# Performance work log

Hardware: AMD Instinct MI355X
Metric: run time of the kernel (lower is better)

## Reference

```python
import jax, jax.numpy as jnp
import numpy as np


def setup_inputs() -> dict:
    key = jax.random.key(0)
    ks = jax.random.split(key, 7)
    B, N, D, A = 32, 128, 512, 512
    sD = 1.0 / np.sqrt(D)
    sA = 1.0 / np.sqrt(A)
    return {
        "x": jax.random.normal(ks[0], (B, N, D), dtype=jnp.float32),
        "W1": jax.random.normal(ks[1], (A, D), dtype=jnp.float32) * sD,
        "b1": jax.random.normal(ks[2], (A,), dtype=jnp.float32) * sD,
        "W2": jax.random.normal(ks[3], (A, D), dtype=jnp.float32) * sD,
        "b2": jax.random.normal(ks[4], (A,), dtype=jnp.float32) * sD,
        "Wout": jax.random.normal(ks[5], (A,), dtype=jnp.float32) * sA,
        "bout": jax.random.normal(ks[6], (1,), dtype=jnp.float32) * sA,
    }


def reference(x, W1, b1, W2, b2, Wout, bout):
    # x: (B, N, D)
    x1 = jnp.einsum('bnd,ad->bna', x, W1) + b1  # mlp1 -> (B, N, A)
    x2 = jnp.einsum('bnd,ad->bna', x, W2) + b2  # mlp2 -> (B, N, A)
    # outer broadcast add: x1.unsqueeze(1) + x2.unsqueeze(2) -> (B, N, N, A)
    s = x1[:, None, :, :] + x2[:, :, None, :]
    # include_root=False: drop ROOT row along dim 1 -> (B, N-1, N, A)
    s = s[:, 1:, :, :]
    s = jnp.tanh(s)
    # out linear A -> 1, then squeeze -> (B, N-1, N)
    return jnp.einsum('bija,a->bij', s, Wout) + bout[0]
```

## Files before the change

### kernel.cpp

```cpp
#include <hip/hip_runtime.h>
#include <hip/hip_bf16.h>

#define B_ 32
#define N_ 128
#define D_ 512
#define A_ 512
#define R_ (B_*N_)
#define OC 1024
#define CEXP 2.8853900817779268f

typedef __attribute__((ext_vector_type(8)))  short frag_ab;
typedef __attribute__((ext_vector_type(16))) float frag_c;

__device__ inline unsigned pack2bf(float a, float b) {
    unsigned ua = __builtin_bit_cast(unsigned, a) + 0x8000u;
    unsigned ub = __builtin_bit_cast(unsigned, b) + 0x8000u;
    return __builtin_amdgcn_perm(ub, ua, 0x07060302);
}
__device__ inline float bf2f_lo(unsigned u){ return __builtin_bit_cast(float, u << 16); }
__device__ inline float bf2f_hi(unsigned u){ return __builtin_bit_cast(float, u & 0xffff0000u); }

__global__ __launch_bounds__(256) void k0_cvt(
    const float* __restrict__ X, const float* __restrict__ W1,
    const float* __restrict__ W2,
    unsigned short* __restrict__ Xb, unsigned short* __restrict__ W1b,
    unsigned short* __restrict__ W2b)
{
    const int NX = R_*D_/8, NW = A_*D_/8;
    int i = blockIdx.x*256 + threadIdx.x;
    const float* src; unsigned short* dst; int off;
    if (i < NX)            { src = X;  dst = Xb;  off = i; }
    else if (i < NX+NW)    { src = W1; dst = W1b; off = i-NX; }
    else if (i < NX+2*NW)  { src = W2; dst = W2b; off = i-NX-NW; }
    else return;
    float4 a = ((const float4*)src)[off*2];
    float4 c = ((const float4*)src)[off*2+1];
    uint4 o;
    o.x = pack2bf(a.x,a.y); o.y = pack2bf(a.z,a.w);
    o.z = pack2bf(c.x,c.y); o.w = pack2bf(c.z,c.w);
    ((uint4*)dst)[off] = o;
}

#define LDK1 36

__global__ __launch_bounds__(256) void k1_mfma(
    const unsigned short* __restrict__ Xb,
    const unsigned short* __restrict__ W1b, const float* __restrict__ b1,
    const unsigned short* __restrict__ W2b, const float* __restrict__ b2,
    unsigned short* __restrict__ Yb)
{
    __shared__ unsigned short As[2][128*LDK1];
    __shared__ unsigned short Bs[2][128*LDK1];

    const int t = threadIdx.x, lane = t&63, wid = t>>6;
    const int wr = wid>>1, wc = wid&1;
    const int row0 = blockIdx.x*128, col0 = blockIdx.y*128;
    const unsigned short* Wb = (col0 < A_) ? W1b : W2b;
    const float* bb = (col0 < A_) ? b1 : b2;
    const int wrow0 = col0 & (A_-1);

    const int srow = t>>1;
    const int scol = (t&1)*16;

    frag_c acc[2][2];
#pragma unroll
    for (int i=0;i<2;++i)
#pragma unroll
        for (int j=0;j<2;++j)
#pragma unroll
            for (int r=0;r<16;++r) acc[i][j][r] = 0.f;

    const int fr = lane & 31;
    const int ko = (lane >> 5) * 8;

    {
        const unsigned short* px = &Xb[(size_t)(row0 +srow)*D_ + scol];
        const unsigned short* pw = &Wb[(size_t)(wrow0+srow)*D_ + scol];
        uint4 a0 = *(const uint4*)px, a1 = *(const uint4*)(px+8);
        uint4 b0 = *(const uint4*)pw, b1v = *(const uint4*)(pw+8);
        *(uint4*)&As[0][srow*LDK1 + scol]     = a0;
        *(uint4*)&As[0][srow*LDK1 + scol + 8] = a1;
        *(uint4*)&Bs[0][srow*LDK1 + scol]     = b0;
        *(uint4*)&Bs[0][srow*LDK1 + scol + 8] = b1v;
    }
    __syncthreads();

#pragma unroll
    for (int s = 0; s < 16; ++s) {
        const int cur = s & 1;
        uint4 a0, a1, b0, b1v;
        if (s < 15) {
            const int k0 = (s+1)*32;
            const unsigned short* px = &Xb[(size_t)(row0 +srow)*D_ + k0 + scol];
            const unsigned short* pw = &Wb[(size_t)(wrow0+srow)*D_ + k0 + scol];
            a0 = *(const uint4*)px; a1 = *(const uint4*)(px+8);
            b0 = *(const uint4*)pw; b1v = *(const uint4*)(pw+8);
        }
        frag_ab af[2][2], bf[2][2];
#pragma unroll
        for (int mt=0; mt<2; ++mt)
#pragma unroll
            for (int ks=0; ks<2; ++ks) {
                af[mt][ks] = *(const frag_ab*)&As[cur][(wr*64+mt*32+fr)*LDK1 + ks*16 + ko];
                bf[mt][ks] = *(const frag_ab*)&Bs[cur][(wc*64+mt*32+fr)*LDK1 + ks*16 + ko];
            }
#pragma unroll
        for (int ks=0; ks<2; ++ks)
#pragma unroll
            for (int mt=0; mt<2; ++mt)
#pragma unroll
                for (int nt=0; nt<2; ++nt)
                    acc[mt][nt] = __builtin_amdgcn_mfma_f32_32x32x16_bf16(
                        af[mt][ks], bf[nt][ks], acc[mt][nt], 0, 0, 0);
        if (s < 15) {
            *(uint4*)&As[cur^1][srow*LDK1 + scol]     = a0;
            *(uint4*)&As[cur^1][srow*LDK1 + scol + 8] = a1;
            *(uint4*)&Bs[cur^1][srow*LDK1 + scol]     = b0;
            *(uint4*)&Bs[cur^1][srow*LDK1 + scol + 8] = b1v;
        }
        __syncthreads();
    }

#pragma unroll
    for (int mt=0; mt<2; ++mt) {
        const int rbase = row0 + wr*64 + mt*32 + 4*(lane>>5);
#pragma unroll
        for (int nt=0; nt<2; ++nt) {
            const int cc = col0 + wc*64 + nt*32 + (lane&31);
            const float bias = bb[cc & (A_-1)];
#pragma unroll
            for (int r=0; r<16; ++r) {
                const int rr = rbase + (r&3) + 8*(r>>2);
                float e = __builtin_amdgcn_exp2f(CEXP*(acc[mt][nt][r] + bias));
                Yb[(size_t)rr*OC + cc] =
                    (unsigned short)((__builtin_bit_cast(unsigned, e) + 0x8000u) >> 16);
            }
        }
    }
}

#define LDW 132

__device__ inline int swz(int r, int c) { return r*LDW + (c ^ (((r>>2)&7)<<2)); }

__global__ __launch_bounds__(256) void k2_tanh(
    const unsigned short* __restrict__ Yb,
    const float* __restrict__ Wout, const float* __restrict__ bout,
    float* __restrict__ out)
{
    __shared__ float e1s[64*LDW];
    __shared__ float e2s[64*LDW];
    __shared__ float wo[128];
    __shared__ float wsum_s[4];

    const int t  = threadIdx.x;
    const int jt = blockIdx.x & 1;
    const int it = blockIdx.x >> 1;
    const int ah = blockIdx.y;
    const int b  = blockIdx.z;
    const int abase = ah << 7;

    {
        float w = (t < 128) ? Wout[abase + t] : 0.f;
        if (t < 128) wo[t] = w;
#pragma unroll
        for (int off=32; off>=1; off>>=1) w += __shfl_down(w, off, 64);
        if ((t&63)==0) wsum_s[t>>6] = w;
    }

    const unsigned short* yb = Yb + (size_t)b*N_*OC;
    const int sr = t>>4;
    const int sc = (t&15)*8;

#pragma unroll
    for (int q=0; q<4; ++q) {
        const int r = q*16 + sr;
        uint4 v1 = *(const uint4*)&yb[(size_t)(jt*64 + r)*OC + abase + sc];
        int i2 = it*64 + r + 1; if (i2 > 127) i2 = 127;
        uint4 v2 = *(const uint4*)&yb[(size_t)i2*OC + A_ + abase + sc];
        *(float4*)&e1s[swz(r, sc)]   = float4{bf2f_lo(v1.x),bf2f_hi(v1.x),bf2f_lo(v1.y),bf2f_hi(v1.y)};
        *(float4*)&e1s[swz(r, sc+4)] = float4{bf2f_lo(v1.z),bf2f_hi(v1.z),bf2f_lo(v1.w),bf2f_hi(v1.w)};
        *(float4*)&e2s[swz(r, sc)]   = float4{bf2f_lo(v2.x),bf2f_hi(v2.x),bf2f_lo(v2.y),bf2f_hi(v2.y)};
        *(float4*)&e2s[swz(r, sc+4)] = float4{bf2f_lo(v2.z),bf2f_hi(v2.z),bf2f_lo(v2.w),bf2f_hi(v2.w)};
    }
    __syncthreads();

    const int jl = t&15, il = t>>4;
    float acc[4][4];
#pragma unroll
    for (int kj=0;kj<4;++kj)
#pragma unroll
        for (int ki=0;ki<4;++ki) acc[kj][ki] = 0.f;

#pragma unroll 1
    for (int c=0; c<128; c+=4) {
        float4 u[4], v[4];
#pragma unroll
        for (int kj=0;kj<4;++kj) u[kj] = *(const float4*)&e1s[swz(4*jl+kj, c)];
#pragma unroll
        for (int ki=0;ki<4;++ki) v[ki] = *(const float4*)&e2s[swz(4*il+ki, c)];
        float4 w4 = *(const float4*)&wo[c];
#pragma unroll
        for (int kj=0;kj<4;++kj)
#pragma unroll
            for (int ki=0;ki<4;++ki) {
                float r0 = fmaf(u[kj].x, v[ki].x, 1.f);
                float s0 = fmaf(u[kj].y, v[ki].y, 1.f);
                acc[kj][ki] = fmaf(fmaf(w4.x, s0, w4.y*r0),
                                   __builtin_amdgcn_rcpf(r0*s0), acc[kj][ki]);
                float r1 = fmaf(u[kj].z, v[ki].z, 1.f);
                float s1 = fmaf(u[kj].w, v[ki].w, 1.f);
                acc[kj][ki] = fmaf(fmaf(w4.z, s1, w4.w*r1),
                                   __builtin_amdgcn_rcpf(r1*s1), acc[kj][ki]);
            }
    }

    const float wsum = wsum_s[0]+wsum_s[1]+wsum_s[2]+wsum_s[3];
    const float base = wsum + (ah ? 0.f : bout[0]);
    float* ob = out + (size_t)b*127*128;
#pragma unroll
    for (int ki=0;ki<4;++ki) {
        const int i0 = it*64 + 4*il + ki;
        if (i0 < 127) {
#pragma unroll
            for (int kj=0;kj<4;++kj) {
                const int j0 = jt*64 + 4*jl + kj;
                atomicAdd(&ob[i0*128 + j0], base - 2.f*acc[kj][ki]);
            }
        }
    }
}

extern "C" void kernel_launch(void* const* d_in, const int* in_sizes, int n_in,
                              void* d_out, int out_size, void* d_ws, size_t ws_size,
                              hipStream_t stream) {
    const float* x    = (const float*)d_in[0];
    const float* W1   = (const float*)d_in[1];
    const float* b1   = (const float*)d_in[2];
    const float* W2   = (const float*)d_in[3];
    const float* b2   = (const float*)d_in[4];
    const float* Wout = (const float*)d_in[5];
    const float* bout = (const float*)d_in[6];
    float* out = (float*)d_out;

    char* ws = (char*)d_ws;
    unsigned short* Yb  = (unsigned short*)ws;
    unsigned short* Xb  = (unsigned short*)(ws + (8u<<20));
    unsigned short* W1b = (unsigned short*)(ws + (12u<<20));
    unsigned short* W2b = (unsigned short*)(ws + (12u<<20) + (1u<<19));

    k0_cvt<<<1280, 256, 0, stream>>>(x, W1, W2, Xb, W1b, W2b);

    dim3 g1(R_/128, OC/128);
    k1_mfma<<<g1, 256, 0, stream>>>(Xb, W1b, b1, W2b, b2, Yb);

    hipMemsetAsync(d_out, 0, (size_t)out_size*sizeof(float), stream);

    dim3 g2(4, 4, B_);
    k2_tanh<<<g2, 256, 0, stream>>>(Yb, Wout, bout, out);
}
```

Measured before the change: 131.8 us.

## Shrink GEMM tiles, split tanh kernel by A-chunks, replace atomics with reduction

The projection GEMM moves to 64x64 tiles with a K-step of 64 and an XOR-swizzled LDS layout, so more blocks are launched. The pairwise tanh kernel keeps e1/e2 in LDS as bf16 and splits A into eight 64-wide chunks, doubling its grid. Each chunk writes partial sums to a workspace buffer instead of using atomics. A new reduce kernel sums the eight partials and adds the bias, which removes the memset and atomic contention. The cost is an extra launch plus partial-buffer traffic, and bf16 unpacking now happens in the inner loop.

Result: faster. 122.9 us (-6.7%).

```diff
diff --git a/kernel.cpp b/kernel.cpp
--- a/kernel.cpp
+++ b/kernel.cpp
@@ -41,194 +41,198 @@
     ((uint4*)dst)[off] = o;
 }
 
-#define LDK1 36
-
 __global__ __launch_bounds__(256) void k1_mfma(
     const unsigned short* __restrict__ Xb,
     const unsigned short* __restrict__ W1b, const float* __restrict__ b1,
     const unsigned short* __restrict__ W2b, const float* __restrict__ b2,
     unsigned short* __restrict__ Yb)
 {
-    __shared__ unsigned short As[2][128*LDK1];
-    __shared__ unsigned short Bs[2][128*LDK1];
+    __shared__ unsigned short As[2][64*64];
+    __shared__ unsigned short Bs[2][64*64];
 
     const int t = threadIdx.x, lane = t&63, wid = t>>6;
     const int wr = wid>>1, wc = wid&1;
-    const int row0 = blockIdx.x*128, col0 = blockIdx.y*128;
+    const int row0 = blockIdx.x*64, col0 = blockIdx.y*64;
     const unsigned short* Wb = (col0 < A_) ? W1b : W2b;
     const float* bb = (col0 < A_) ? b1 : b2;
     const int wrow0 = col0 & (A_-1);
 
-    const int srow = t>>1;
-    const int scol = (t&1)*16;
-
-    frag_c acc[2][2];
-#pragma unroll
-    for (int i=0;i<2;++i)
-#pragma unroll
-        for (int j=0;j<2;++j)
-#pragma unroll
-            for (int r=0;r<16;++r) acc[i][j][r] = 0.f;
+    const int sr = t>>2;
+    const int ss = (t&3)*2;
+    const int sf = sr & 7;
+
+    frag_c acc;
+#pragma unroll
+    for (int r=0;r<16;++r) acc[r] = 0.f;
 
     const int fr = lane & 31;
-    const int ko = (lane >> 5) * 8;
+    const int hs = lane >> 5;
+    const int arow = wr*32 + fr, af_f = arow & 7;
+    const int brow = wc*32 + fr, bf_f = brow & 7;
 
     {
-        const unsigned short* px = &Xb[(size_t)(row0 +srow)*D_ + scol];
-        const unsigned short* pw = &Wb[(size_t)(wrow0+srow)*D_ + scol];
+        const unsigned short* px = &Xb[(size_t)(row0 +sr)*D_ + ss*8];
+        const unsigned short* pw = &Wb[(size_t)(wrow0+sr)*D_ + ss*8];
         uint4 a0 = *(const uint4*)px, a1 = *(const uint4*)(px+8);
         uint4 b0 = *(const uint4*)pw, b1v = *(const uint4*)(pw+8);
-        *(uint4*)&As[0][srow*LDK1 + scol]     = a0;
-        *(uint4*)&As[0][srow*LDK1 + scol + 8] = a1;
-        *(uint4*)&Bs[0][srow*LDK1 + scol]     = b0;
-        *(uint4*)&Bs[0][srow*LDK1 + scol + 8] = b1v;
+        *(uint4*)&As[0][sr*64 + (( ss   ^sf)<<3)] = a0;
+        *(uint4*)&As[0][sr*64 + (((ss+1)^sf)<<3)] = a1;
+        *(uint4*)&Bs[0][sr*64 + (( ss   ^sf)<<3)] = b0;
+        *(uint4*)&Bs[0][sr*64 + (((ss+1)^sf)<<3)] = b1v;
     }
     __syncthreads();
 
 #pragma unroll
-    for (int s = 0; s < 16; ++s) {
+    for (int s = 0; s < 8; ++s) {
         const int cur = s & 1;
         uint4 a0, a1, b0, b1v;
-        if (s < 15) {
-            const int k0 = (s+1)*32;
-            const unsigned short* px = &Xb[(size_t)(row0 +srow)*D_ + k0 + scol];
-            const unsigned short* pw = &Wb[(size_t)(wrow0+srow)*D_ + k0 + scol];
+        if (s < 7) {
+            const int k0 = (s+1)*64;
+            const unsigned short* px = &Xb[(size_t)(row0 +sr)*D_ + k0 + ss*8];
+            const unsigned short* pw = &Wb[(size_t)(wrow0+sr)*D_ + k0 + ss*8];
             a0 = *(const uint4*)px; a1 = *(const uint4*)(px+8);
             b0 = *(const uint4*)pw; b1v = *(const uint4*)(pw+8);
         }
-        frag_ab af[2][2], bf[2][2];
-#pragma unroll
-        for (int mt=0; mt<2; ++mt)
-#pragma unroll
-            for (int ks=0; ks<2; ++ks) {
-                af[mt][ks] = *(const frag_ab*)&As[cur][(wr*64+mt*32+fr)*LDK1 + ks*16 + ko];
-                bf[mt][ks] = *(const frag_ab*)&Bs[cur][(wc*64+mt*32+fr)*LDK1 + ks*16 + ko];
-            }
-#pragma unroll
-        for (int ks=0; ks<2; ++ks)
-#pragma unroll
-            for (int mt=0; mt<2; ++mt)
-#pragma unroll
-                for (int nt=0; nt<2; ++nt)
-                    acc[mt][nt] = __builtin_amdgcn_mfma_f32_32x32x16_bf16(
-                        af[mt][ks], bf[nt][ks], acc[mt][nt], 0, 0, 0);
-        if (s < 15) {
-            *(uint4*)&As[cur^1][srow*LDK1 + scol]     = a0;
-            *(uint4*)&As[cur^1][srow*LDK1 + scol + 8] = a1;
-            *(uint4*)&Bs[cur^1][srow*LDK1 + scol]     = b0;
-            *(uint4*)&Bs[cur^1][srow*LDK1 + scol + 8] = b1v;
+        frag_ab af[4], bf[4];
+#pragma unroll
+        for (int ks=0; ks<4; ++ks) {
+            const int slot = ks*2 + hs;
+            af[ks] = *(const frag_ab*)&As[cur][arow*64 + ((slot^af_f)<<3)];
+            bf[ks] = *(const frag_ab*)&Bs[cur][brow*64 + ((slot^bf_f)<<3)];
+        }
+#pragma unroll
+        for (int ks=0; ks<4; ++ks)
+            acc = __builtin_amdgcn_mfma_f32_32x32x16_bf16(af[ks], bf[ks], acc, 0, 0, 0);
+        if (s < 7) {
+            *(uint4*)&As[cur^1][sr*64 + (( ss   ^sf)<<3)] = a0;
+            *(uint4*)&As[cur^1][sr*64 + (((ss+1)^sf)<<3)] = a1;
+            *(uint4*)&Bs[cur^1][sr*64 + (( ss   ^sf)<<3)] = b0;
+            *(uint4*)&Bs[cur^1][sr*64 + (((ss+1)^sf)<<3)] = b1v;
         }
         __syncthreads();
     }
 
-#pragma unroll
-    for (int mt=0; mt<2; ++mt) {
-        const int rbase = row0 + wr*64 + mt*32 + 4*(lane>>5);
-#pragma unroll
-        for (int nt=0; nt<2; ++nt) {
-            const int cc = col0 + wc*64 + nt*32 + (lane&31);
-            const float bias = bb[cc & (A_-1)];
-#pragma unroll
-            for (int r=0; r<16; ++r) {
-                const int rr = rbase + (r&3) + 8*(r>>2);
-                float e = __builtin_amdgcn_exp2f(CEXP*(acc[mt][nt][r] + bias));
-                Yb[(size_t)rr*OC + cc] =
-                    (unsigned short)((__builtin_bit_cast(unsigned, e) + 0x8000u) >> 16);
-            }
-        }
-    }
-}
-
-#define LDW 132
-
-__device__ inline int swz(int r, int c) { return r*LDW + (c ^ (((r>>2)&7)<<2)); }
+    const int cc = col0 + wc*32 + (lane&31);
+    const float bias = bb[cc & (A_-1)];
+    const int rbase = row0 + wr*32 + 4*(lane>>5);
+#pragma unroll
+    for (int r=0; r<16; ++r) {
+        const int rr = rbase + (r&3) + 8*(r>>2);
+        float e = __builtin_amdgcn_exp2f(CEXP*(acc[r] + bias));
+        Yb[(size_t)rr*OC + cc] =
+            (unsigned short)((__builtin_bit_cast(unsigned, e) + 0x8000u) >> 16);
+    }
+}
 
 __global__ __launch_bounds__(256) void k2_tanh(
     const unsigned short* __restrict__ Yb,
-    const float* __restrict__ Wout, const float* __restrict__ bout,
-    float* __restrict__ out)
-{
-    __shared__ float e1s[64*LDW];
-    __shared__ float e2s[64*LDW];
-    __shared__ float wo[128];
-    __shared__ float wsum_s[4];
+    const float* __restrict__ Wout,
+    float* __restrict__ P)
+{
+    __shared__ unsigned short e1s[64*64];
+    __shared__ unsigned short e2s[64*64];
+    __shared__ float wo[64];
+    __shared__ float wsum_s;
 
     const int t  = threadIdx.x;
     const int jt = blockIdx.x & 1;
     const int it = blockIdx.x >> 1;
-    const int ah = blockIdx.y;
+    const int ac = blockIdx.y;
     const int b  = blockIdx.z;
-    const int abase = ah << 7;
-
+    const int abase = ac*64;
+
+    if (t < 64) {
+        float w = Wout[abase + t];
+        wo[t] = w;
+#pragma unroll
+        for (int off=32; off>=1; off>>=1) w += __shfl_down(w, off, 64);
+        if (t == 0) wsum_s = w;
+    }
+
+    const unsigned short* yb = Yb + (size_t)b*N_*OC;
     {
-        float w = (t < 128) ? Wout[abase + t] : 0.f;
-        if (t < 128) wo[t] = w;
-#pragma unroll
-        for (int off=32; off>=1; off>>=1) w += __shfl_down(w, off, 64);
-        if ((t&63)==0) wsum_s[t>>6] = w;
-    }
-
-    const unsigned short* yb = Yb + (size_t)b*N_*OC;
-    const int sr = t>>4;
-    const int sc = (t&15)*8;
-
-#pragma unroll
-    for (int q=0; q<4; ++q) {
-        const int r = q*16 + sr;
-        uint4 v1 = *(const uint4*)&yb[(size_t)(jt*64 + r)*OC + abase + sc];
-        int i2 = it*64 + r + 1; if (i2 > 127) i2 = 127;
-        uint4 v2 = *(const uint4*)&yb[(size_t)i2*OC + A_ + abase + sc];
-        *(float4*)&e1s[swz(r, sc)]   = float4{bf2f_lo(v1.x),bf2f_hi(v1.x),bf2f_lo(v1.y),bf2f_hi(v1.y)};
-        *(float4*)&e1s[swz(r, sc+4)] = float4{bf2f_lo(v1.z),bf2f_hi(v1.z),bf2f_lo(v1.w),bf2f_hi(v1.w)};
-        *(float4*)&e2s[swz(r, sc)]   = float4{bf2f_lo(v2.x),bf2f_hi(v2.x),bf2f_lo(v2.y),bf2f_hi(v2.y)};
-        *(float4*)&e2s[swz(r, sc+4)] = float4{bf2f_lo(v2.z),bf2f_hi(v2.z),bf2f_lo(v2.w),bf2f_hi(v2.w)};
+        const int r  = t>>2;
+        const int s0 = (t&3)*2;
+        const int f  = (r>>2)&7;
+        int g2 = it*64 + r + 1; if (g2 > 127) g2 = 127;
+        const unsigned short* p1 = &yb[(size_t)(jt*64 + r)*OC + abase + s0*8];
+        const unsigned short* p2 = &yb[(size_t)g2*OC + A_ + abase + s0*8];
+        uint4 a0 = *(const uint4*)p1, a1 = *(const uint4*)(p1+8);
+        uint4 b0 = *(const uint4*)p2, b1v = *(const uint4*)(p2+8);
+        *(uint4*)&e1s[r*64 + (( s0   ^f)<<3)] = a0;
+        *(uint4*)&e1s[r*64 + (((s0+1)^f)<<3)] = a1;
+        *(uint4*)&e2s[r*64 + (( s0   ^f)<<3)] = b0;
+        *(uint4*)&e2s[r*64 + (((s0+1)^f)<<3)] = b1v;
     }
     __syncthreads();
 
     const int jl = t&15, il = t>>4;
+    const int fj = jl&7, fi = il&7;
     float acc[4][4];
 #pragma unroll
     for (int kj=0;kj<4;++kj)
 #pragma unroll
         for (int ki=0;ki<4;++ki) acc[kj][ki] = 0.f;
 
-#pragma unroll 1
-    for (int c=0; c<128; c+=4) {
-        float4 u[4], v[4];
-#pragma unroll
-        for (int kj=0;kj<4;++kj) u[kj] = *(const float4*)&e1s[swz(4*jl+kj, c)];
-#pragma unroll
-        for (int ki=0;ki<4;++ki) v[ki] = *(const float4*)&e2s[swz(4*il+ki, c)];
-        float4 w4 = *(const float4*)&wo[c];
-#pragma unroll
-        for (int kj=0;kj<4;++kj)
+#pragma unroll
+    for (int c8=0; c8<8; ++c8) {
+        uint4 V4[4];
+#pragma unroll
+        for (int ki=0;ki<4;++ki)
+            V4[ki] = *(const uint4*)&e2s[(4*il+ki)*64 + ((c8^fi)<<3)];
+        float vf[4][8];
+#pragma unroll
+        for (int ki=0;ki<4;++ki) {
+            vf[ki][0]=bf2f_lo(V4[ki].x); vf[ki][1]=bf2f_hi(V4[ki].x);
+            vf[ki][2]=bf2f_lo(V4[ki].y); vf[ki][3]=bf2f_hi(V4[ki].y);
+            vf[ki][4]=bf2f_lo(V4[ki].z); vf[ki][5]=bf2f_hi(V4[ki].z);
+            vf[ki][6]=bf2f_lo(V4[ki].w); vf[ki][7]=bf2f_hi(V4[ki].w);
+        }
+        float4 wa = *(const float4*)&wo[c8*8];
+        float4 wb = *(const float4*)&wo[c8*8 + 4];
+#pragma unroll
+        for (int kj=0;kj<4;++kj) {
+            uint4 U = *(const uint4*)&e1s[(4*jl+kj)*64 + ((c8^fj)<<3)];
+            float u0=bf2f_lo(U.x), u1=bf2f_hi(U.x), u2=bf2f_lo(U.y), u3=bf2f_hi(U.y);
+            float u4=bf2f_lo(U.z), u5=bf2f_hi(U.z), u6=bf2f_lo(U.w), u7=bf2f_hi(U.w);
 #pragma unroll
             for (int ki=0;ki<4;++ki) {
-                float r0 = fmaf(u[kj].x, v[ki].x, 1.f);
-                float s0 = fmaf(u[kj].y, v[ki].y, 1.f);
-                acc[kj][ki] = fmaf(fmaf(w4.x, s0, w4.y*r0),
-                                   __builtin_amdgcn_rcpf(r0*s0), acc[kj][ki]);
-                float r1 = fmaf(u[kj].z, v[ki].z, 1.f);
-                float s1 = fmaf(u[kj].w, v[ki].w, 1.f);
-                acc[kj][ki] = fmaf(fmaf(w4.z, s1, w4.w*r1),
-                                   __builtin_amdgcn_rcpf(r1*s1), acc[kj][ki]);
+                { float r0=fmaf(u0,vf[ki][0],1.f), s0=fmaf(u1,vf[ki][1],1.f);
+                  acc[kj][ki]=fmaf(fmaf(wa.x,s0,wa.y*r0),__builtin_amdgcn_rcpf(r0*s0),acc[kj][ki]); }
+                { float r0=fmaf(u2,vf[ki][2],1.f), s0=fmaf(u3,vf[ki][3],1.f);
+                  acc[kj][ki]=fmaf(fmaf(wa.z,s0,wa.w*r0),__builtin_amdgcn_rcpf(r0*s0),acc[kj][ki]); }
+                { float r0=fmaf(u4,vf[ki][4],1.f), s0=fmaf(u5,vf[ki][5],1.f);
+                  acc[kj][ki]=fmaf(fmaf(wb.x,s0,wb.y*r0),__builtin_amdgcn_rcpf(r0*s0),acc[kj][ki]); }
+                { float r0=fmaf(u6,vf[ki][6],1.f), s0=fmaf(u7,vf[ki][7],1.f);
+                  acc[kj][ki]=fmaf(fmaf(wb.z,s0,wb.w*r0),__builtin_amdgcn_rcpf(r0*s0),acc[kj][ki]); }
             }
-    }
-
-    const float wsum = wsum_s[0]+wsum_s[1]+wsum_s[2]+wsum_s[3];
-    const float base = wsum + (ah ? 0.f : bout[0]);
-    float* ob = out + (size_t)b*127*128;
+        }
+    }
+
+    const float base = wsum_s;
+    float* Pb = P + ((size_t)(ac*B_ + b))*128*128;
 #pragma unroll
     for (int ki=0;ki<4;++ki) {
         const int i0 = it*64 + 4*il + ki;
-        if (i0 < 127) {
-#pragma unroll
-            for (int kj=0;kj<4;++kj) {
-                const int j0 = jt*64 + 4*jl + kj;
-                atomicAdd(&ob[i0*128 + j0], base - 2.f*acc[kj][ki]);
-            }
-        }
-    }
+        float4 o = { base - 2.f*acc[0][ki], base - 2.f*acc[1][ki],
+                     base - 2.f*acc[2][ki], base - 2.f*acc[3][ki] };
+        *(float4*)&Pb[i0*128 + jt*64 + 4*jl] = o;
+    }
+}
+
+__global__ __launch_bounds__(256) void k3_reduce(
+    const float* __restrict__ P, const float* __restrict__ bout,
+    float* __restrict__ out)
+{
+    int o = blockIdx.x*256 + threadIdx.x;
+    if (o >= B_*127*128) return;
+    const int b = o / (127*128);
+    const int rem = o - b*127*128;
+    const float* p = P + (size_t)b*16384 + rem;
+    float s = bout[0];
+#pragma unroll
+    for (int q=0; q<8; ++q) s += p[(size_t)q*B_*16384];
+    out[o] = s;
 }
 
 extern "C" void kernel_launch(void* const* d_in, const int* in_sizes, int n_in,
@@ -248,14 +252,15 @@
     unsigned short* Xb  = (unsigned short*)(ws + (8u<<20));
     unsigned short* W1b = (unsigned short*)(ws + (12u<<20));
     unsigned short* W2b = (unsigned short*)(ws + (12u<<20) + (1u<<19));
+    float*          P   = (float*)(ws + (16u<<20));
 
     k0_cvt<<<1280, 256, 0, stream>>>(x, W1, W2, Xb, W1b, W2b);
 
-    dim3 g1(R_/128, OC/128);
+    dim3 g1(R_/64, OC/64);
     k1_mfma<<<g1, 256, 0, stream>>>(Xb, W1b, b1, W2b, b2, Yb);
 
-    hipMemsetAsync(d_out, 0, (size_t)out_size*sizeof(float), stream);
-
-    dim3 g2(4, 4, B_);
-    k2_tanh<<<g2, 256, 0, stream>>>(Yb, Wout, bout, out);
-}
+    dim3 g2(4, 8, B_);
+    k2_tanh<<<g2, 256, 0, stream>>>(Yb, Wout, P);
+
+    k3_reduce<<<(B_*127*128 + 255)/256, 256, 0, stream>>>(P, bout, out);
+}
```
